# Kernel optimization log

Measured on AMD Instinct MI355X. Metric: run time of the kernel, lower is better.

## Reference

```python
import jax, jax.numpy as jnp
import numpy as np

B, E, N, D, L = 16, 1024, 2048, 256, 3


def setup_inputs() -> dict:
    key = jax.random.key(0)
    ks = jax.random.split(key, 8)
    return {
        "evidences_mat": jax.random.normal(ks[0], (B, E, D), jnp.float32),
        "entities_mat": jax.random.normal(ks[1], (B, N, D), jnp.float32),
        "ev_to_ent": jax.random.bernoulli(ks[2], 0.05, (B, E, N)).astype(jnp.float32),
        "ent_to_ev": jax.random.bernoulli(ks[3], 0.05, (B, N, E)).astype(jnp.float32),
        "w_weight": jax.random.normal(ks[4], (L, D, D), jnp.float32) * 0.05,
        "w_bias": jax.random.normal(ks[5], (L, D), jnp.float32) * 0.05,
        "watt_weight": jax.random.normal(ks[6], (L, D, D), jnp.float32) * 0.05,
        "watt_bias": jax.random.normal(ks[7], (L, D), jnp.float32) * 0.05,
    }


def reference(evidences_mat, entities_mat, ev_to_ent, ent_to_ev,
              w_weight, w_bias, watt_weight, watt_bias):
    ev, ent = evidences_mat, entities_mat
    for i in range(L):
        # attention projections (torch Linear: x @ W.T + b)
        pe = jnp.einsum('bed,od->beo', ev, watt_weight[i]) + watt_bias[i]   # [B,E,D]
        pn = jnp.einsum('bnd,od->bno', ent, watt_weight[i]) + watt_bias[i]  # [B,N,D]
        # evidences -> entities messages
        ev_att = jnp.einsum('bed,bnd->ben', pe, pn) * ev_to_ent             # [B,E,N]
        ev_att = jax.nn.softmax(ev_att, axis=1)                              # over E (dim=1)
        msg_ent = jnp.einsum('ben,bed->bnd', ev_att, ev)                     # [B,N,D]
        msg_ent = jnp.einsum('bnd,od->bno', msg_ent, w_weight[i]) + w_bias[i]
        self_ent = jnp.einsum('bnd,od->bno', ent, w_weight[i]) + w_bias[i]
        ent = jax.nn.relu(msg_ent + self_ent)
        # entities -> evidences messages (uses UPDATED entities, as in source)
        ent_att = jnp.einsum('bnd,bed->bne', pn, pe) * ent_to_ev            # [B,N,E]
        ent_att = jax.nn.softmax(ent_att, axis=1)                            # over N (dim=1)
        msg_ev = jnp.einsum('bne,bnd->bed', ent_att, ent)                    # [B,E,D]
        msg_ev = jnp.einsum('bed,od->beo', msg_ev, w_weight[i]) + w_bias[i]
        self_ev = jnp.einsum('bed,od->beo', ev, w_weight[i]) + w_bias[i]
        ev = jax.nn.relu(msg_ev + self_ev)
        # dropout is a no-op (p=0.0 / eval)
    return ent, ev
```

## Files before the change

### kernel.cpp

```cpp
#include <hip/hip_runtime.h>

#define BB 16
#define EE 1024
#define NN 2048
#define DD 256
#define LL 3

typedef _Float16 half8 __attribute__((ext_vector_type(8)));
typedef _Float16 half4 __attribute__((ext_vector_type(4)));
typedef _Float16 half2_t __attribute__((ext_vector_type(2)));
typedef float f32x4 __attribute__((ext_vector_type(4)));

__device__ __forceinline__ void pmerge(float& m, float& s, float m2, float s2) {
    float nm = fmaxf(m, m2);
    s = s * __expf(m - nm) + s2 * __expf(m2 - nm);
    m = nm;
}

__device__ __forceinline__ unsigned pk2(_Float16 a, _Float16 b) {
    union { _Float16 h[2]; unsigned u; } x;
    x.h[0] = a; x.h[1] = b;
    return x.u;
}

__global__ void split_cast(const float* __restrict__ in, _Float16* __restrict__ hi,
                           _Float16* __restrict__ lo, size_t n) {
    size_t stride = (size_t)gridDim.x * blockDim.x * 4;
    for (size_t i = ((size_t)blockIdx.x * blockDim.x + threadIdx.x) * 4; i < n; i += stride) {
        float4 v = *(const float4*)&in[i];
        half4 hh, ll;
        _Float16 h;
        h = (_Float16)v.x; hh[0] = h; ll[0] = (_Float16)(v.x - (float)h);
        h = (_Float16)v.y; hh[1] = h; ll[1] = (_Float16)(v.y - (float)h);
        h = (_Float16)v.z; hh[2] = h; ll[2] = (_Float16)(v.z - (float)h);
        h = (_Float16)v.w; hh[3] = h; ll[3] = (_Float16)(v.w - (float)h);
        *(half4*)&hi[i] = hh;
        *(half4*)&lo[i] = ll;
    }
}

__global__ void cast_u8(const float* __restrict__ in, unsigned char* __restrict__ out, size_t n) {
    size_t stride = (size_t)gridDim.x * blockDim.x * 4;
    for (size_t i = ((size_t)blockIdx.x * blockDim.x + threadIdx.x) * 4; i < n; i += stride) {
        float4 v = *(const float4*)&in[i];
        unsigned int pack = (unsigned int)(unsigned char)v.x |
                            ((unsigned int)(unsigned char)v.y << 8) |
                            ((unsigned int)(unsigned char)v.z << 16) |
                            ((unsigned int)(unsigned char)v.w << 24);
        *(unsigned int*)&out[i] = pack;
    }
}

__global__ void transpose_split(const float* __restrict__ in, _Float16* __restrict__ oh,
                                _Float16* __restrict__ olo, int R, int C) {
    int b = blockIdx.z;
    int c0 = blockIdx.x * 64, r0 = blockIdx.y * 64;
    const float* ib = in + (size_t)b * R * C;
    size_t ob = (size_t)b * R * C;
    __shared__ float tile[64][65];
    int t = threadIdx.x;
    int cl = t & 63, rb = t >> 6;
#pragma unroll
    for (int j = 0; j < 16; j++) {
        int rl = rb + j * 4;
        tile[rl][cl] = ib[(size_t)(r0 + rl) * C + c0 + cl];
    }
    __syncthreads();
    int oc = t >> 2, q = t & 3;
    half8 h0, h1, l0, l1;
#pragma unroll
    for (int i = 0; i < 8; i++) {
        float v = tile[q * 16 + i][oc];
        _Float16 h = (_Float16)v;
        h0[i] = h; l0[i] = (_Float16)(v - (float)h);
    }
#pragma unroll
    for (int i = 0; i < 8; i++) {
        float v = tile[q * 16 + 8 + i][oc];
        _Float16 h = (_Float16)v;
        h1[i] = h; l1[i] = (_Float16)(v - (float)h);
    }
    size_t o = ob + (size_t)(c0 + oc) * R + r0 + q * 16;
    *(half8*)&oh[o] = h0; *(half8*)&oh[o + 8] = h1;
    *(half8*)&olo[o] = l0; *(half8*)&olo[o + 8] = l1;
}

__global__ void transpose_split_perm(const float* __restrict__ in, _Float16* __restrict__ oh,
                                     _Float16* __restrict__ olo, int R, int C) {
    int b = blockIdx.z;
    int c0 = blockIdx.x * 64, r0 = blockIdx.y * 64;
    const float* ib = in + (size_t)b * R * C;
    size_t ob = (size_t)b * R * C;
    __shared__ float tile[64][65];
    int t = threadIdx.x;
    int cl = t & 63, rb = t >> 6;
#pragma unroll
    for (int j = 0; j < 16; j++) {
        int rl = rb + j * 4;
        tile[rl][cl] = ib[(size_t)(r0 + rl) * C + c0 + cl];
    }
    __syncthreads();
    int oc = t >> 2, q = t & 3;
    int g = q >> 1, sub = q & 1;
#pragma unroll
    for (int j = 0; j < 8; j++) {
        int x = sub * 8 + j;
        float v1 = tile[g * 32 + x][oc];
        float v2 = tile[g * 32 + x + 16][oc];
        _Float16 a = (_Float16)v1, b2 = (_Float16)v2;
        _Float16 la = (_Float16)(v1 - (float)a), lb = (_Float16)(v2 - (float)b2);
        size_t o = ob + (size_t)(c0 + oc) * R + r0 + g * 32 + 2 * x;
        half2_t hp; hp[0] = a; hp[1] = b2;
        half2_t lp; lp[0] = la; lp[1] = lb;
        *(half2_t*)&oh[o] = hp;
        *(half2_t*)&olo[o] = lp;
    }
}

__global__ void transpose_u8(const float* __restrict__ in, unsigned char* __restrict__ out,
                             int R, int C) {
    int b = blockIdx.z;
    int c0 = blockIdx.x * 64, r0 = blockIdx.y * 64;
    const float* ib = in + (size_t)b * R * C;
    unsigned char* ob = out + (size_t)b * R * C;
    __shared__ float tile[64][65];
    int t = threadIdx.x;
    int cl = t & 63, rb = t >> 6;
#pragma unroll
    for (int j = 0; j < 16; j++) {
        int rl = rb + j * 4;
        tile[rl][cl] = ib[(size_t)(r0 + rl) * C + c0 + cl];
    }
    __syncthreads();
    int oc = t >> 2, q = t & 3;
    union { unsigned char b[16]; uint4 v; } u;
#pragma unroll
    for (int i = 0; i < 16; i++) u.b[i] = (unsigned char)tile[q * 16 + i][oc];
    size_t o = (size_t)(c0 + oc) * R + r0 + q * 16;
    *(uint4*)&ob[o] = u.v;
}

template <bool A_SPLIT, bool B_SPLIT, bool HAS_BIAS, bool RELU, bool HAS_ADD,
          bool WRITE_F32, bool WRITE_SPLIT, bool B_BATCHED>
__global__ __launch_bounds__(256) void gemm_nt(
    const _Float16* __restrict__ Ah, const _Float16* __restrict__ Al,
    const _Float16* __restrict__ Bh, const _Float16* __restrict__ Bl,
    const float* __restrict__ bias, float bscale,
    const float* __restrict__ addsrc,
    float* __restrict__ Cf, _Float16* __restrict__ Chi, _Float16* __restrict__ Clo,
    int M, int Nn, int K) {
    const int bz = blockIdx.z;
    const int m0 = blockIdx.x * 128, n0 = blockIdx.y * 128;
    const int t = threadIdx.x, lane = t & 63, wid = t >> 6;
    const int wm = wid >> 1, wn = wid & 1;
    const size_t offA = (size_t)bz * M * K;
    const size_t offB = B_BATCHED ? (size_t)bz * Nn * K : (size_t)0;
    const _Float16* Abh = Ah + offA;
    const _Float16* Abl = A_SPLIT ? (Al + offA) : nullptr;
    const _Float16* Bbh = Bh + offB;
    const _Float16* Bbl = B_SPLIT ? (Bl + offB) : nullptr;

    __shared__ _Float16 sAh[128 * 32];
    __shared__ _Float16 sBh[128 * 32];
    __shared__ _Float16 sAl[A_SPLIT ? 128 * 32 : 1];
    __shared__ _Float16 sBl[B_SPLIT ? 128 * 32 : 1];

    f32x4 acc[4][4] = {};
    const int nk = K >> 5;

    auto gA = [&](const _Float16* base, int kt, int q) {
        return *(const uint4*)(base + (size_t)(m0 + (q >> 2)) * K + (kt << 5) + ((q & 3) << 3));
    };
    auto gB = [&](const _Float16* base, int kt, int q) {
        return *(const uint4*)(base + (size_t)(n0 + (q >> 2)) * K + (kt << 5) + ((q & 3) << 3));
    };

    uint4 rah0 = gA(Abh, 0, t), rah1 = gA(Abh, 0, t + 256);
    uint4 rbh0 = gB(Bbh, 0, t), rbh1 = gB(Bbh, 0, t + 256);
    uint4 ral0 = {}, ral1 = {}, rbl0 = {}, rbl1 = {};
    if (A_SPLIT) { ral0 = gA(Abl, 0, t); ral1 = gA(Abl, 0, t + 256); }
    if (B_SPLIT) { rbl0 = gB(Bbl, 0, t); rbl1 = gB(Bbl, 0, t + 256); }

    for (int kt = 0; kt < nk; ++kt) {
        __syncthreads();
        ((uint4*)sAh)[t] = rah0; ((uint4*)sAh)[t + 256] = rah1;
        ((uint4*)sBh)[t] = rbh0; ((uint4*)sBh)[t + 256] = rbh1;
        if (A_SPLIT) { ((uint4*)sAl)[t] = ral0; ((uint4*)sAl)[t + 256] = ral1; }
        if (B_SPLIT) { ((uint4*)sBl)[t] = rbl0; ((uint4*)sBl)[t + 256] = rbl1; }
        __syncthreads();
        if (kt + 1 < nk) {
            rah0 = gA(Abh, kt + 1, t); rah1 = gA(Abh, kt + 1, t + 256);
            rbh0 = gB(Bbh, kt + 1, t); rbh1 = gB(Bbh, kt + 1, t + 256);
            if (A_SPLIT) { ral0 = gA(Abl, kt + 1, t); ral1 = gA(Abl, kt + 1, t + 256); }
            if (B_SPLIT) { rbl0 = gB(Bbl, kt + 1, t); rbl1 = gB(Bbl, kt + 1, t + 256); }
        }
        half8 afh[4], bfh[4], afl[4], bfl[4];
#pragma unroll
        for (int mi = 0; mi < 4; mi++) {
            int off = (wm * 64 + mi * 16 + (lane & 15)) * 32 + ((lane >> 4) << 3);
            afh[mi] = *(const half8*)&sAh[off];
            if (A_SPLIT) afl[mi] = *(const half8*)&sAl[off];
        }
#pragma unroll
        for (int nj = 0; nj < 4; nj++) {
            int off = (wn * 64 + nj * 16 + (lane & 15)) * 32 + ((lane >> 4) << 3);
            bfh[nj] = *(const half8*)&sBh[off];
            if (B_SPLIT) bfl[nj] = *(const half8*)&sBl[off];
        }
#pragma unroll
        for (int mi = 0; mi < 4; mi++)
#pragma unroll
            for (int nj = 0; nj < 4; nj++) {
                acc[mi][nj] = __builtin_amdgcn_mfma_f32_16x16x32_f16(afh[mi], bfh[nj], acc[mi][nj], 0, 0, 0);
                if (B_SPLIT)
                    acc[mi][nj] = __builtin_amdgcn_mfma_f32_16x16x32_f16(afh[mi], bfl[nj], acc[mi][nj], 0, 0, 0);
                if (A_SPLIT)
                    acc[mi][nj] = __builtin_amdgcn_mfma_f32_16x16x32_f16(afl[mi], bfh[nj], acc[mi][nj], 0, 0, 0);
            }
    }

    const int rbase = (lane >> 4) * 4, cc = lane & 15;
#pragma unroll
    for (int mi = 0; mi < 4; mi++) {
#pragma unroll
        for (int nj = 0; nj < 4; nj++) {
            int gn = n0 + wn * 64 + nj * 16 + cc;
            float bv = HAS_BIAS ? bias[gn] * bscale : 0.f;
#pragma unroll
            for (int r = 0; r < 4; r++) {
                int gm = m0 + wm * 64 + mi * 16 + rbase + r;
                float v = acc[mi][nj][r];
                if (HAS_BIAS) v += bv;
                size_t off = ((size_t)bz * M + gm) * Nn + gn;
                if (HAS_ADD) v += addsrc[off];
                if (RELU) v = fmaxf(v, 0.f);
                if (WRITE_F32) Cf[off] = v;
                if (WRITE_SPLIT) {
                    _Float16 h = (_Float16)v;
                    Chi[off] = h;
                    Clo[off] = (_Float16)(v - (float)h);
                }
            }
        }
    }
}

template <bool TRANSA>
__global__ __launch_bounds__(256) void fused_agg(
    const float* __restrict__ S_, const unsigned char* __restrict__ Mk,
    const float2* __restrict__ st, const _Float16* __restrict__ Bh,
    const _Float16* __restrict__ Bl, const float* __restrict__ addsrc,
    _Float16* __restrict__ Xhi, _Float16* __restrict__ Xlo,
    int M, int K) {
    const int bz = blockIdx.z;
    const int m0 = blockIdx.x * 64, n0 = blockIdx.y * 128;
    const int t = threadIdx.x, lane = t & 63, wid = t >> 6;
    const int wm = wid >> 1, wn = wid & 1;
    const float* Sb = S_ + (size_t)bz * EE * NN;
    const unsigned char* Mb = Mk + (size_t)bz * EE * NN;
    const float2* stb = st + (size_t)bz * M;
    const _Float16* Bbh = Bh + (size_t)bz * DD * K;
    const _Float16* Bbl = Bl + (size_t)bz * DD * K;

    __shared__ _Float16 sA[64 * 32];
    __shared__ _Float16 sBh[128 * 32];
    __shared__ _Float16 sBl[128 * 32];

    f32x4 acc[2][4] = {};
    const int nk = K >> 5;

    float stc[4], stem[4];
    if (TRANSA) {
        int ncol = (t & 15) * 4;
#pragma unroll
        for (int i = 0; i < 4; i++) {
            float2 v = stb[m0 + ncol + i];
            stc[i] = v.x; stem[i] = v.y;
        }
    } else {
#pragma unroll
        for (int p = 0; p < 2; p++) {
            float2 v = stb[m0 + (t >> 3) + p * 32];
            stc[p] = v.x; stem[p] = v.y;
        }
    }

    struct RawA { f32x4 s1, s2; unsigned a1, a2; };
    RawA A0, A1;
    uint4 rbh0, rbh1, rbl0, rbl1;

    auto prefA_load = [&](RawA& R, int kt) {
        if (TRANSA) {
            int r = t >> 4, ncol = (t & 15) * 4;
            size_t rowoff = (size_t)(kt * 32 + r) * NN + m0 + ncol;
            R.s1 = *(const f32x4*)(Sb + rowoff);
            R.s2 = *(const f32x4*)(Sb + rowoff + (size_t)16 * NN);
            R.a1 = *(const unsigned*)(Mb + rowoff);
            R.a2 = *(const unsigned*)(Mb + rowoff + (size_t)16 * NN);
        } else {
            int kc = (t & 7) * 4, rb = t >> 3;
            size_t ro1 = (size_t)(m0 + rb) * NN + kt * 32 + kc;
            size_t ro2 = (size_t)(m0 + rb + 32) * NN + kt * 32 + kc;
            R.s1 = *(const f32x4*)(Sb + ro1);
            R.s2 = *(const f32x4*)(Sb + ro2);
            R.a1 = *(const unsigned*)(Mb + ro1);
            R.a2 = *(const unsigned*)(Mb + ro2);
        }
    };
    auto prefB = [&](int kt) {
        auto g = [&](const _Float16* base, int q) {
            return *(const uint4*)(base + (size_t)(n0 + (q >> 2)) * K + kt * 32 + (q & 3) * 8);
        };
        rbh0 = g(Bbh, t); rbh1 = g(Bbh, t + 256);
        rbl0 = g(Bbl, t); rbl1 = g(Bbl, t + 256);
    };
    auto storeA = [&](RawA& R) {
        if (TRANSA) {
            int r = t >> 4, ncol = (t & 15) * 4;
#pragma unroll
            for (int i = 0; i < 4; i++) {
                float c = stc[i], em = stem[i];
                float x1 = ((R.a1 >> (8 * i)) & 255u) ? __expf(R.s1[i] - c) : em;
                float x2 = ((R.a2 >> (8 * i)) & 255u) ? __expf(R.s2[i] - c) : em;
                int n = ncol + i;
                int cp = (r >> 2) ^ ((n >> 2) & 3);
                ((unsigned*)sA)[n * 16 + cp * 4 + (r & 3)] = pk2((_Float16)x1, (_Float16)x2);
            }
        } else {
            int kc = (t & 7) * 4, rb = t >> 3;
            {
                float c = stc[0], em = stem[0];
                _Float16 h0 = (_Float16)(((R.a1) & 255u) ? __expf(R.s1[0] - c) : em);
                _Float16 h1 = (_Float16)(((R.a1 >> 8) & 255u) ? __expf(R.s1[1] - c) : em);
                _Float16 h2 = (_Float16)(((R.a1 >> 16) & 255u) ? __expf(R.s1[2] - c) : em);
                _Float16 h3 = (_Float16)(((R.a1 >> 24) & 255u) ? __expf(R.s1[3] - c) : em);
                unsigned* dst = (unsigned*)&sA[rb * 32 + kc];
                dst[0] = pk2(h0, h1); dst[1] = pk2(h2, h3);
            }
            {
                float c = stc[1], em = stem[1];
                _Float16 h0 = (_Float16)(((R.a2) & 255u) ? __expf(R.s2[0] - c) : em);
                _Float16 h1 = (_Float16)(((R.a2 >> 8) & 255u) ? __expf(R.s2[1] - c) : em);
                _Float16 h2 = (_Float16)(((R.a2 >> 16) & 255u) ? __expf(R.s2[2] - c) : em);
                _Float16 h3 = (_Float16)(((R.a2 >> 24) & 255u) ? __expf(R.s2[3] - c) : em);
                unsigned* dst = (unsigned*)&sA[(rb + 32) * 32 + kc];
                dst[0] = pk2(h0, h1); dst[1] = pk2(h2, h3);
            }
        }
    };
    auto storeB = [&]() {
        ((uint4*)sBh)[t] = rbh0; ((uint4*)sBh)[t + 256] = rbh1;
        ((uint4*)sBl)[t] = rbl0; ((uint4*)sBl)[t + 256] = rbl1;
    };
    auto compute = [&]() {
        half8 af[2], bfh[4], bfl[4];
        const int l4 = lane & 15, h = lane >> 4;
        const int cswz = TRANSA ? (h ^ ((l4 >> 2) & 3)) : h;
#pragma unroll
        for (int mi = 0; mi < 2; mi++)
            af[mi] = *(const half8*)&sA[(wm * 32 + mi * 16 + l4) * 32 + cswz * 8];
#pragma unroll
        for (int nj = 0; nj < 4; nj++) {
            int off = (wn * 64 + nj * 16 + l4) * 32 + h * 8;
            bfh[nj] = *(const half8*)&sBh[off];
            bfl[nj] = *(const half8*)&sBl[off];
        }
#pragma unroll
        for (int mi = 0; mi < 2; mi++)
#pragma unroll
            for (int nj = 0; nj < 4; nj++) {
                acc[mi][nj] = __builtin_amdgcn_mfma_f32_16x16x32_f16(af[mi], bfh[nj], acc[mi][nj], 0, 0, 0);
                acc[mi][nj] = __builtin_amdgcn_mfma_f32_16x16x32_f16(af[mi], bfl[nj], acc[mi][nj], 0, 0, 0);
            }
    };

    prefA_load(A0, 0);
    prefA_load(A1, 1);
    prefB(0);

    for (int kt = 0; kt < nk; kt += 2) {
        __syncthreads();
        storeA(A0); storeB();
        __syncthreads();
        if (kt + 2 < nk) prefA_load(A0, kt + 2);
        prefB(kt + 1);
        compute();
        __syncthreads();
        storeA(A1); storeB();
        __syncthreads();
        if (kt + 3 < nk) prefA_load(A1, kt + 3);
        if (kt + 2 < nk) prefB(kt + 2);
        compute();
    }

    const int rbase = (lane >> 4) * 4, cc = lane & 15;
#pragma unroll
    for (int mi = 0; mi < 2; mi++) {
#pragma unroll
        for (int nj = 0; nj < 4; nj++) {
            int gn = n0 + wn * 64 + nj * 16 + cc;
#pragma unroll
            for (int r = 0; r < 4; r++) {
                int gm = m0 + wm * 32 + mi * 16 + rbase + r;
                size_t off = ((size_t)bz * M + gm) * DD + gn;
                float v = acc[mi][nj][r] + addsrc[off];
                _Float16 h = (_Float16)v;
                Xhi[off] = h;
                Xlo[off] = (_Float16)(v - (float)h);
            }
        }
    }
}

__global__ __launch_bounds__(256) void stats(const float* __restrict__ S_,
                                             const unsigned char* __restrict__ m1,
                                             const unsigned char* __restrict__ m2t,
                                             float2* __restrict__ d1p,
                                             float2* __restrict__ d2p) {
    int b = blockIdx.z, e0 = blockIdx.y * 64, n0 = blockIdx.x * 256;
    int t = threadIdx.x, lane = t & 63, w = t >> 6;
    size_t base = ((size_t)b * EE + e0) * NN + n0;

    f32x4 xs[16];
    unsigned int am[16], cm[16];
#pragma unroll
    for (int j = 0; j < 16; j++) {
        size_t off = base + (size_t)(w * 16 + j) * NN + lane * 4;
        float4 s = *(const float4*)(S_ + off);
        xs[j][0] = s.x; xs[j][1] = s.y; xs[j][2] = s.z; xs[j][3] = s.w;
        am[j] = *(const unsigned int*)(m1 + off);
        cm[j] = *(const unsigned int*)(m2t + off);
    }

    float cmx[4], csm[4];
#pragma unroll
    for (int i = 0; i < 4; i++) {
        float mx = ((am[0] >> (8 * i)) & 0xffu) ? xs[0][i] : 0.f;
#pragma unroll
        for (int j = 1; j < 16; j++) {
            float xe = ((am[j] >> (8 * i)) & 0xffu) ? xs[j][i] : 0.f;
            mx = fmaxf(mx, xe);
        }
        float sm = 0.f;
#pragma unroll
        for (int j = 0; j < 16; j++) {
            float xe = ((am[j] >> (8 * i)) & 0xffu) ? xs[j][i] : 0.f;
            sm += __expf(xe - mx);
        }
        cmx[i] = mx; csm[i] = sm;
    }
    __shared__ float rm[4][256], rs[4][256];
#pragma unroll
    for (int i = 0; i < 4; i++) { rm[w][lane * 4 + i] = cmx[i]; rs[w][lane * 4 + i] = csm[i]; }
    __syncthreads();
    {
        float M0 = rm[0][t], S0 = rs[0][t];
#pragma unroll
        for (int ww = 1; ww < 4; ww++) pmerge(M0, S0, rm[ww][t], rs[ww][t]);
        d1p[(size_t)blockIdx.y * (BB * NN) + (size_t)b * NN + n0 + t] = make_float2(M0, S0);
    }

#pragma unroll
    for (int j = 0; j < 16; j++) {
        float x0 = ((cm[j]) & 0xffu) ? xs[j][0] : 0.f;
        float x1 = ((cm[j] >> 8) & 0xffu) ? xs[j][1] : 0.f;
        float x2 = ((cm[j] >> 16) & 0xffu) ? xs[j][2] : 0.f;
        float x3 = ((cm[j] >> 24) & 0xffu) ? xs[j][3] : 0.f;
        float mx = fmaxf(fmaxf(x0, x1), fmaxf(x2, x3));
#pragma unroll
        for (int off = 1; off < 64; off <<= 1) mx = fmaxf(mx, __shfl_xor(mx, off, 64));
        float sm = __expf(x0 - mx) + __expf(x1 - mx) + __expf(x2 - mx) + __expf(x3 - mx);
#pragma unroll
        for (int off = 1; off < 64; off <<= 1) sm += __shfl_xor(sm, off, 64);
        if (lane == 0)
            d2p[(size_t)blockIdx.x * (BB * EE) + (size_t)b * EE + e0 + w * 16 + j] = make_float2(mx, sm);
    }
}

__global__ void reduce_dens(const float2* __restrict__ d1p, const float2* __restrict__ d2p,
                            float2* __restrict__ d1, float2* __restrict__ d2) {
    int i = blockIdx.x * 256 + threadIdx.x;
    if (i < BB * NN) {
        float2 v = d1p[i];
        float m = v.x, s = v.y;
#pragma unroll
        for (int k = 1; k < 16; k++) {
            float2 u = d1p[(size_t)k * (BB * NN) + i];
            pmerge(m, s, u.x, u.y);
        }
        float c = m + __logf(s);
        d1[i] = make_float2(c, __expf(-c));
    } else {
        int j = i - BB * NN;
        if (j < BB * EE) {
            float2 v = d2p[j];
            float m = v.x, s = v.y;
#pragma unroll
            for (int k = 1; k < 8; k++) {
                float2 u = d2p[(size_t)k * (BB * EE) + j];
                pmerge(m, s, u.x, u.y);
            }
            float c = m + __logf(s);
            d2[j] = make_float2(c, __expf(-c));
        }
    }
}

extern "C" void kernel_launch(void* const* d_in, const int* in_sizes, int n_in,
                              void* d_out, int out_size, void* d_ws, size_t ws_size,
                              hipStream_t stream) {
    const float* evid   = (const float*)d_in[0];
    const float* enti   = (const float*)d_in[1];
    const float* ev2ent = (const float*)d_in[2];
    const float* ent2ev = (const float*)d_in[3];
    const float* w_w    = (const float*)d_in[4];
    const float* w_b    = (const float*)d_in[5];
    const float* wa_w   = (const float*)d_in[6];
    const float* wa_b   = (const float*)d_in[7];
    float* out_ent = (float*)d_out;
    float* out_ev  = out_ent + (size_t)BB * NN * DD;

    char* p = (char*)d_ws;
    auto alloc = [&](size_t bytes) {
        char* r = p;
        p += (bytes + 255) & ~(size_t)255;
        return (void*)r;
    };
    const size_t nED = (size_t)BB * EE * DD, nND = (size_t)BB * NN * DD;
    const size_t nEN = (size_t)BB * EE * NN, nW = (size_t)LL * DD * DD;
    _Float16* Whi  = (_Float16*)alloc(nW * 2);
    _Float16* Wlo  = (_Float16*)alloc(nW * 2);
    _Float16* Wahi = (_Float16*)alloc(nW * 2);
    _Float16* Walo = (_Float16*)alloc(nW * 2);
    _Float16* evh  = (_Float16*)alloc(nED * 2);
    _Float16* evl  = (_Float16*)alloc(nED * 2);
    _Float16* enth = (_Float16*)alloc(nND * 2);
    _Float16* entl = (_Float16*)alloc(nND * 2);
    _Float16* evTh = (_Float16*)alloc(nED * 2);
    _Float16* evTl = (_Float16*)alloc(nED * 2);
    _Float16* entTh= (_Float16*)alloc(nND * 2);
    _Float16* entTl= (_Float16*)alloc(nND * 2);
    _Float16* peh  = (_Float16*)alloc(nED * 2);
    _Float16* pel  = (_Float16*)alloc(nED * 2);
    _Float16* pnh  = (_Float16*)alloc(nND * 2);
    _Float16* pnl  = (_Float16*)alloc(nND * 2);
    float*    S    = (float*)alloc(nEN * 4);
    unsigned char* m1  = (unsigned char*)alloc(nEN);
    unsigned char* m2t = (unsigned char*)alloc(nEN);
    float* evS  = (float*)alloc(nED * 4);
    float* entS = (float*)alloc(nND * 4);
    float2* d1p = (float2*)alloc((size_t)16 * BB * NN * 8);
    float2* d2p = (float2*)alloc((size_t)8 * BB * EE * 8);
    float2* d1  = (float2*)alloc((size_t)BB * NN * 8);
    float2* d2  = (float2*)alloc((size_t)BB * EE * 8);
    if ((size_t)(p - (char*)d_ws) > ws_size) return;
    _Float16* Xenth = pnh; _Float16* Xentl = pnl;
    _Float16* Xevh  = peh; _Float16* Xevl  = pel;

    split_cast<<<2048, 256, 0, stream>>>(wa_w, Wahi, Walo, nW);
    split_cast<<<2048, 256, 0, stream>>>(w_w, Whi, Wlo, nW);
    split_cast<<<2048, 256, 0, stream>>>(evid, evh, evl, nED);
    split_cast<<<2048, 256, 0, stream>>>(enti, enth, entl, nND);
    cast_u8<<<2048, 256, 0, stream>>>(ev2ent, m1, nEN);
    transpose_u8<<<dim3(EE / 64, NN / 64, BB), 256, 0, stream>>>(ent2ev, m2t, NN, EE);
    transpose_split_perm<<<dim3(DD / 64, EE / 64, BB), 256, 0, stream>>>(evid, evTh, evTl, EE, DD);
    hipMemcpyAsync(evS, evid, nED * 4, hipMemcpyDeviceToDevice, stream);
    hipMemcpyAsync(entS, enti, nND * 4, hipMemcpyDeviceToDevice, stream);

    for (int i = 0; i < LL; i++) {
        const _Float16* Wih  = Whi + (size_t)i * DD * DD;
        const _Float16* Wil  = Wlo + (size_t)i * DD * DD;
        const _Float16* Waih = Wahi + (size_t)i * DD * DD;
        const _Float16* Wail = Walo + (size_t)i * DD * DD;
        const float* bi  = w_b + i * DD;
        const float* bai = wa_b + i * DD;

        gemm_nt<true, true, true, false, false, false, true, false>
            <<<dim3(EE / 128, DD / 128, BB), 256, 0, stream>>>(
                evh, evl, Waih, Wail, bai, 1.f, nullptr, nullptr, peh, pel, EE, DD, DD);
        gemm_nt<true, true, true, false, false, false, true, false>
            <<<dim3(NN / 128, DD / 128, BB), 256, 0, stream>>>(
                enth, entl, Waih, Wail, bai, 1.f, nullptr, nullptr, pnh, pnl, NN, DD, DD);
        gemm_nt<true, true, false, false, false, true, false, true>
            <<<dim3(EE / 128, NN / 128, BB), 256, 0, stream>>>(
                peh, pel, pnh, pnl, nullptr, 0.f, nullptr, S, nullptr, nullptr, EE, NN, DD);
        stats<<<dim3(NN / 256, EE / 64, BB), 256, 0, stream>>>(S, m1, m2t, d1p, d2p);
        reduce_dens<<<(BB * NN + BB * EE + 255) / 256, 256, 0, stream>>>(d1p, d2p, d1, d2);
        fused_agg<true><<<dim3(NN / 64, 2, BB), 256, 0, stream>>>(
            S, m1, d1, evTh, evTl, entS, Xenth, Xentl, NN, EE);
        float* entDst = (i == LL - 1) ? out_ent : entS;
        gemm_nt<true, true, true, true, false, true, true, false>
            <<<dim3(NN / 128, DD / 128, BB), 256, 0, stream>>>(
                Xenth, Xentl, Wih, Wil, bi, 2.f, nullptr, entDst, enth, entl, NN, DD, DD);
        transpose_split<<<dim3(DD / 64, NN / 64, BB), 256, 0, stream>>>(entDst, entTh, entTl, NN, DD);
        fused_agg<false><<<dim3(EE / 64, 2, BB), 256, 0, stream>>>(
            S, m2t, d2, entTh, entTl, evS, Xevh, Xevl, EE, NN);
        float* evDst = (i == LL - 1) ? out_ev : evS;
        gemm_nt<true, true, true, true, false, true, true, false>
            <<<dim3(EE / 128, DD / 128, BB), 256, 0, stream>>>(
                Xevh, Xevl, Wih, Wil, bi, 2.f, nullptr, evDst, evh, evl, EE, DD, DD);
        if (i < LL - 1)
            transpose_split_perm<<<dim3(DD / 64, EE / 64, BB), 256, 0, stream>>>(evS, evTh, evTl, EE, DD);
    }
}
```

Before: 1.367 ms.

## Fuse masked softmax statistics into score GEMM epilogue

Removes the separate stats kernel, which re-read the full fp32 score matrix and both masks. The score GEMM now computes partial column max/sum (over E) and row max/sum (over N) from its accumulator registers, using wave shuffles, and writes them to the partial buffers. The number of row partials grows from 8 to 32, so reduce_dens and the d2p allocation are enlarged. The epilogue still does scattered byte reads of both masks and adds register pressure to the GEMM.

```diff
diff --git a/kernel.cpp b/kernel.cpp
--- a/kernel.cpp
+++ b/kernel.cpp
@@ -141,13 +141,15 @@
 }
 
 template <bool A_SPLIT, bool B_SPLIT, bool HAS_BIAS, bool RELU, bool HAS_ADD,
-          bool WRITE_F32, bool WRITE_SPLIT, bool B_BATCHED>
+          bool WRITE_F32, bool WRITE_SPLIT, bool B_BATCHED, bool COMPUTE_STATS>
 __global__ __launch_bounds__(256) void gemm_nt(
     const _Float16* __restrict__ Ah, const _Float16* __restrict__ Al,
     const _Float16* __restrict__ Bh, const _Float16* __restrict__ Bl,
     const float* __restrict__ bias, float bscale,
     const float* __restrict__ addsrc,
     float* __restrict__ Cf, _Float16* __restrict__ Chi, _Float16* __restrict__ Clo,
+    const unsigned char* __restrict__ Mk1, const unsigned char* __restrict__ Mk2,
+    float2* __restrict__ d1p, float2* __restrict__ d2p,
     int M, int Nn, int K) {
     const int bz = blockIdx.z;
     const int m0 = blockIdx.x * 128, n0 = blockIdx.y * 128;
@@ -242,6 +244,85 @@
                 }
             }
         }
+    }
+
+    if (COMPUTE_STATS) {
+        unsigned long long mb1 = 0ull, mb2 = 0ull;
+#pragma unroll
+        for (int mi = 0; mi < 4; mi++)
+#pragma unroll
+            for (int nj = 0; nj < 4; nj++)
+#pragma unroll
+                for (int r = 0; r < 4; r++) {
+                    int gm = m0 + wm * 64 + mi * 16 + rbase + r;
+                    int gn = n0 + wn * 64 + nj * 16 + cc;
+                    size_t off = ((size_t)bz * M + gm) * Nn + gn;
+                    int idx = mi * 16 + nj * 4 + r;
+                    if (Mk1[off]) mb1 |= 1ull << idx;
+                    if (Mk2[off]) mb2 |= 1ull << idx;
+                }
+#pragma unroll
+        for (int nj = 0; nj < 4; nj++) {
+            float mx = -1e30f;
+#pragma unroll
+            for (int mi = 0; mi < 4; mi++)
+#pragma unroll
+                for (int r = 0; r < 4; r++) {
+                    int idx = mi * 16 + nj * 4 + r;
+                    float xe = ((mb1 >> idx) & 1ull) ? acc[mi][nj][r] : 0.f;
+                    mx = fmaxf(mx, xe);
+                }
+            float sm = 0.f;
+#pragma unroll
+            for (int mi = 0; mi < 4; mi++)
+#pragma unroll
+                for (int r = 0; r < 4; r++) {
+                    int idx = mi * 16 + nj * 4 + r;
+                    float xe = ((mb1 >> idx) & 1ull) ? acc[mi][nj][r] : 0.f;
+                    sm += __expf(xe - mx);
+                }
+#pragma unroll
+            for (int s = 16; s < 64; s <<= 1) {
+                float m2 = __shfl_xor(mx, s, 64);
+                float s2 = __shfl_xor(sm, s, 64);
+                pmerge(mx, sm, m2, s2);
+            }
+            if ((lane >> 4) == 0) {
+                int gn = n0 + wn * 64 + nj * 16 + cc;
+                d1p[((size_t)((m0 >> 7) * 2 + wm)) * (BB * NN) + (size_t)bz * NN + gn] =
+                    make_float2(mx, sm);
+            }
+        }
+#pragma unroll
+        for (int mi = 0; mi < 4; mi++)
+#pragma unroll
+            for (int r = 0; r < 4; r++) {
+                float mx = -1e30f;
+#pragma unroll
+                for (int nj = 0; nj < 4; nj++) {
+                    int idx = mi * 16 + nj * 4 + r;
+                    float xe = ((mb2 >> idx) & 1ull) ? acc[mi][nj][r] : 0.f;
+                    mx = fmaxf(mx, xe);
+                }
+                float sm = 0.f;
+#pragma unroll
+                for (int nj = 0; nj < 4; nj++) {
+                    int idx = mi * 16 + nj * 4 + r;
+                    float xe = ((mb2 >> idx) & 1ull) ? acc[mi][nj][r] : 0.f;
+                    sm += __expf(xe - mx);
+                }
+#pragma unroll
+                for (int s = 1; s < 16; s <<= 1) {
+                    float m2 = __shfl_xor(mx, s, 64);
+                    float s2 = __shfl_xor(sm, s, 64);
+                    pmerge(mx, sm, m2, s2);
+                }
+                if (cc == 0) {
+                    int gm = m0 + wm * 64 + mi * 16 + rbase + r;
+                    d2p[((size_t)((n0 >> 7) * 2 + wn)) * (BB * EE) + (size_t)bz * EE + gm] =
+                        make_float2(mx, sm);
+                }
+            }
     }
 }
 
@@ -412,71 +493,6 @@
     }
 }
 
-__global__ __launch_bounds__(256) void stats(const float* __restrict__ S_,
-                                             const unsigned char* __restrict__ m1,
-                                             const unsigned char* __restrict__ m2t,
-                                             float2* __restrict__ d1p,
-                                             float2* __restrict__ d2p) {
-    int b = blockIdx.z, e0 = blockIdx.y * 64, n0 = blockIdx.x * 256;
-    int t = threadIdx.x, lane = t & 63, w = t >> 6;
-    size_t base = ((size_t)b * EE + e0) * NN + n0;
-
-    f32x4 xs[16];
-    unsigned int am[16], cm[16];
-#pragma unroll
-    for (int j = 0; j < 16; j++) {
-        size_t off = base + (size_t)(w * 16 + j) * NN + lane * 4;
-        float4 s = *(const float4*)(S_ + off);
-        xs[j][0] = s.x; xs[j][1] = s.y; xs[j][2] = s.z; xs[j][3] = s.w;
-        am[j] = *(const unsigned int*)(m1 + off);
-        cm[j] = *(const unsigned int*)(m2t + off);
-    }
-
-    float cmx[4], csm[4];
-#pragma unroll
-    for (int i = 0; i < 4; i++) {
-        float mx = ((am[0] >> (8 * i)) & 0xffu) ? xs[0][i] : 0.f;
-#pragma unroll
-        for (int j = 1; j < 16; j++) {
-            float xe = ((am[j] >> (8 * i)) & 0xffu) ? xs[j][i] : 0.f;
-            mx = fmaxf(mx, xe);
-        }
-        float sm = 0.f;
-#pragma unroll
-        for (int j = 0; j < 16; j++) {
-            float xe = ((am[j] >> (8 * i)) & 0xffu) ? xs[j][i] : 0.f;
-            sm += __expf(xe - mx);
-        }
-        cmx[i] = mx; csm[i] = sm;
-    }
-    __shared__ float rm[4][256], rs[4][256];
-#pragma unroll
-    for (int i = 0; i < 4; i++) { rm[w][lane * 4 + i] = cmx[i]; rs[w][lane * 4 + i] = csm[i]; }
-    __syncthreads();
-    {
-        float M0 = rm[0][t], S0 = rs[0][t];
-#pragma unroll
-        for (int ww = 1; ww < 4; ww++) pmerge(M0, S0, rm[ww][t], rs[ww][t]);
-        d1p[(size_t)blockIdx.y * (BB * NN) + (size_t)b * NN + n0 + t] = make_float2(M0, S0);
-    }
-
-#pragma unroll
-    for (int j = 0; j < 16; j++) {
-        float x0 = ((cm[j]) & 0xffu) ? xs[j][0] : 0.f;
-        float x1 = ((cm[j] >> 8) & 0xffu) ? xs[j][1] : 0.f;
-        float x2 = ((cm[j] >> 16) & 0xffu) ? xs[j][2] : 0.f;
-        float x3 = ((cm[j] >> 24) & 0xffu) ? xs[j][3] : 0.f;
-        float mx = fmaxf(fmaxf(x0, x1), fmaxf(x2, x3));
-#pragma unroll
-        for (int off = 1; off < 64; off <<= 1) mx = fmaxf(mx, __shfl_xor(mx, off, 64));
-        float sm = __expf(x0 - mx) + __expf(x1 - mx) + __expf(x2 - mx) + __expf(x3 - mx);
-#pragma unroll
-        for (int off = 1; off < 64; off <<= 1) sm += __shfl_xor(sm, off, 64);
-        if (lane == 0)
-            d2p[(size_t)blockIdx.x * (BB * EE) + (size_t)b * EE + e0 + w * 16 + j] = make_float2(mx, sm);
-    }
-}
-
 __global__ void reduce_dens(const float2* __restrict__ d1p, const float2* __restrict__ d2p,
                             float2* __restrict__ d1, float2* __restrict__ d2) {
     int i = blockIdx.x * 256 + threadIdx.x;
@@ -496,7 +512,7 @@
             float2 v = d2p[j];
             float m = v.x, s = v.y;
 #pragma unroll
-            for (int k = 1; k < 8; k++) {
+            for (int k = 1; k < 32; k++) {
                 float2 u = d2p[(size_t)k * (BB * EE) + j];
                 pmerge(m, s, u.x, u.y);
             }
@@ -550,7 +566,7 @@
     float* evS  = (float*)alloc(nED * 4);
     float* entS = (float*)alloc(nND * 4);
     float2* d1p = (float2*)alloc((size_t)16 * BB * NN * 8);
-    float2* d2p = (float2*)alloc((size_t)8 * BB * EE * 8);
+    float2* d2p = (float2*)alloc((size_t)32 * BB * EE * 8);
     float2* d1  = (float2*)alloc((size_t)BB * NN * 8);
     float2* d2  = (float2*)alloc((size_t)BB * EE * 8);
     if ((size_t)(p - (char*)d_ws) > ws_size) return;
@@ -575,30 +591,34 @@
         const float* bi  = w_b + i * DD;
         const float* bai = wa_b + i * DD;
 
-        gemm_nt<true, true, true, false, false, false, true, false>
+        gemm_nt<true, true, true, false, false, false, true, false, false>
             <<<dim3(EE / 128, DD / 128, BB), 256, 0, stream>>>(
-                evh, evl, Waih, Wail, bai, 1.f, nullptr, nullptr, peh, pel, EE, DD, DD);
-        gemm_nt<true, true, true, false, false, false, true, false>
+                evh, evl, Waih, Wail, bai, 1.f, nullptr, nullptr, peh, pel,
+                nullptr, nullptr, nullptr, nullptr, EE, DD, DD);
+        gemm_nt<true, true, true, false, false, false, true, false, false>
             <<<dim3(NN / 128, DD / 128, BB), 256, 0, stream>>>(
-                enth, entl, Waih, Wail, bai, 1.f, nullptr, nullptr, pnh, pnl, NN, DD, DD);
-        gemm_nt<true, true, false, false, false, true, false, true>
+                enth, entl, Waih, Wail, bai, 1.f, nullptr, nullptr, pnh, pnl,
+                nullptr, nullptr, nullptr, nullptr, NN, DD, DD);
+        gemm_nt<true, true, false, false, false, true, false, true, true>
             <<<dim3(EE / 128, NN / 128, BB), 256, 0, stream>>>(
-                peh, pel, pnh, pnl, nullptr, 0.f, nullptr, S, nullptr, nullptr, EE, NN, DD);
-        stats<<<dim3(NN / 256, EE / 64, BB), 256, 0, stream>>>(S, m1, m2t, d1p, d2p);
+                peh, pel, pnh, pnl, nullptr, 0.f, nullptr, S, nullptr, nullptr,
+                m1, m2t, d1p, d2p, EE, NN, DD);
         reduce_dens<<<(BB * NN + BB * EE + 255) / 256, 256, 0, stream>>>(d1p, d2p, d1, d2);
         fused_agg<true><<<dim3(NN / 64, 2, BB), 256, 0, stream>>>(
             S, m1, d1, evTh, evTl, entS, Xenth, Xentl, NN, EE);
         float* entDst = (i == LL - 1) ? out_ent : entS;
-        gemm_nt<true, true, true, true, false, true, true, false>
+        gemm_nt<true, true, true, true, false, true, true, false, false>
             <<<dim3(NN / 128, DD / 128, BB), 256, 0, stream>>>(
-                Xenth, Xentl, Wih, Wil, bi, 2.f, nullptr, entDst, enth, entl, NN, DD, DD);
+                Xenth, Xentl, Wih, Wil, bi, 2.f, nullptr, entDst, enth, entl,
+                nullptr, nullptr, nullptr, nullptr, NN, DD, DD);
         transpose_split<<<dim3(DD / 64, NN / 64, BB), 256, 0, stream>>>(entDst, entTh, entTl, NN, DD);
         fused_agg<false><<<dim3(EE / 64, 2, BB), 256, 0, stream>>>(
             S, m2t, d2, entTh, entTl, evS, Xevh, Xevl, EE, NN);
         float* evDst = (i == LL - 1) ? out_ev : evS;
-        gemm_nt<true, true, true, true, false, true, true, false>
+        gemm_nt<true, true, true, true, false, true, true, false, false>
             <<<dim3(EE / 128, DD / 128, BB), 256, 0, stream>>>(
-                Xevh, Xevl, Wih, Wil, bi, 2.f, nullptr, evDst, evh, evl, EE, DD, DD);
+                Xevh, Xevl, Wih, Wil, bi, 2.f, nullptr, evDst, evh, evl,
+                nullptr, nullptr, nullptr, nullptr, EE, DD, DD);
         if (i < LL - 1)
             transpose_split_perm<<<dim3(DD / 64, EE / 64, BB), 256, 0, stream>>>(evS, evTh, evTl, EE, DD);
     }
```

After: 1.495 ms. +9.4%, slower.
